# Performance work log

Hardware: AMD Instinct MI355X
Metric: run time of the kernel (lower is better)

## Reference

```python
import jax, jax.numpy as jnp
import numpy as np

B, L, D_IN = 32, 200, 64
H = 64          # hidden_size
A = 36          # attention_size
NEG_SLOPE = 0.01  # torch LeakyReLU default


def setup_inputs() -> dict:
    key = jax.random.key(0)
    ks = jax.random.split(key, 7)
    s_ln = 1.0 / np.sqrt(D_IN)
    s_w1 = 1.0 / np.sqrt(3 * H)
    s_w2 = 1.0 / np.sqrt(A)
    return {
        "x": jax.random.normal(ks[0], (B, L, D_IN), dtype=jnp.float32),
        "ln_w": jax.random.uniform(ks[1], (D_IN, H), minval=-s_ln, maxval=s_ln, dtype=jnp.float32),
        "ln_b": jax.random.uniform(ks[2], (H,), minval=-s_ln, maxval=s_ln, dtype=jnp.float32),
        "w1": jax.random.uniform(ks[3], (3 * H, A), minval=-s_w1, maxval=s_w1, dtype=jnp.float32),
        "b1": jax.random.uniform(ks[4], (A,), minval=-s_w1, maxval=s_w1, dtype=jnp.float32),
        "w2": jax.random.uniform(ks[5], (A,), minval=-s_w2, maxval=s_w2, dtype=jnp.float32),
        "b2": jax.random.uniform(ks[6], (), minval=-s_w2, maxval=s_w2, dtype=jnp.float32),
    }


def reference(x, ln_w, ln_b, w1, b1, w2, b2):
    # x: [B, L, D_in] -> h: [B, L, H]
    h = jnp.einsum("bld,dh->blh", x, ln_w) + ln_b
    Ld = h.shape[1]
    Hd = h.shape[-1]
    # The torch code concatenates (x1, x2, x1*x2) where x1[b,i,j]=h[b,j],
    # x2[b,i,j]=h[b,i]. Split w1 accordingly instead of materializing the
    # [B,L,L,3H] concat tensor.
    w1a, w1b, w1c = w1[:Hd], w1[Hd:2 * Hd], w1[2 * Hd:]
    a = jnp.einsum("bjh,ha->bja", h, w1a)          # x1 contribution (depends on j)
    c = jnp.einsum("bih,ha->bia", h, w1b)          # x2 contribution (depends on i)
    cross = jnp.einsum("bih,bjh,ha->bija", h, h, w1c)  # (x1*x2) contribution
    pre = a[:, None, :, :] + c[:, :, None, :] + cross + b1   # [B,L,L,A]
    act = jax.nn.leaky_relu(pre, negative_slope=NEG_SLOPE)
    score = jnp.einsum("bija,a->bij", act, w2) + b2          # [B,L,L]
    mask = jnp.tril(jnp.ones((Ld, Ld), dtype=score.dtype))   # causal (incl. diag)
    score = score * mask
    return jnp.einsum("bij,bjh->bih", score, h)               # [B,L,H]
```

## Files before the change

kernel.cpp:

```cpp
#include <hip/hip_runtime.h>

#define B 32
#define L 200
#define DIN 64
#define H 64
#define A 36

typedef __attribute__((ext_vector_type(8))) short short8;
typedef __attribute__((ext_vector_type(4))) float floatx4;
typedef __attribute__((ext_vector_type(8))) float floatx8;

static __device__ __forceinline__ short f2bf(float f) {
    union { float f; unsigned u; } v; v.f = f;
    unsigned r = (v.u + 0x7FFF + ((v.u >> 16) & 1)) >> 16;
    return (short)r;
}

__global__ __launch_bounds__(256) void prep_kernel(
    const float* __restrict__ x, const float* __restrict__ ln_w,
    const float* __restrict__ ln_b, const float* __restrict__ w1,
    float* __restrict__ h_out, float* __restrict__ cc_out, short* __restrict__ hb16_out,
    float* __restrict__ w1a_r, float* __restrict__ w1c_r)
{
    int wave = threadIdx.x >> 6;
    int lane = threadIdx.x & 63;
    int bl = __builtin_amdgcn_readfirstlane(blockIdx.x * 4 + wave);
    const float* xr = x + (size_t)bl * DIN;
    float p0 = ln_b[lane], p1 = 0.f;
    #pragma unroll
    for (int d = 0; d < DIN; d += 2) {
        p0 = fmaf(xr[d],     ln_w[d * H + lane],       p0);
        p1 = fmaf(xr[d + 1], ln_w[(d + 1) * H + lane], p1);
    }
    float acc = p0 + p1;
    __shared__ float hrow[4][H];
    hrow[wave][lane] = acc;
    h_out[(size_t)bl * H + lane] = acc;
    int j = bl % L;
    hb16_out[(size_t)bl * H + (lane ^ ((j & 7) << 3))] = f2bf(acc);
    if (lane < A) {
        float s0 = 0.f, s1 = 0.f;
        #pragma unroll
        for (int hh = 0; hh < H; hh += 2) {
            s0 = fmaf(hrow[wave][hh],     w1[(H + hh) * A + lane],     s0);
            s1 = fmaf(hrow[wave][hh + 1], w1[(H + hh + 1) * A + lane], s1);
        }
        cc_out[(size_t)bl * A + lane] = s0 + s1;
    }
    if (blockIdx.x == 0) {
        for (int idx = threadIdx.x; idx < 2 * 3 * 64 * 8; idx += 256) {
            int e = idx & 7, ln = (idx >> 3) & 63, sn = idx >> 9;
            int s = sn / 3, n = sn - 3 * s;
            int k = s * 32 + (ln >> 4) * 8 + e;
            int c = n * 16 + (ln & 15);
            w1a_r[idx] = (c < A) ? w1[k * A + c] : 0.f;
            w1c_r[idx] = (c < A) ? w1[(2 * H + k) * A + c] : 0.f;
        }
    }
}

__global__ __launch_bounds__(256) void score_kernel(
    const float* __restrict__ h, const short* __restrict__ hb16,
    const float* __restrict__ cc, const float* __restrict__ w1a_r,
    const float* __restrict__ w1c_r, const float* __restrict__ b1,
    const float* __restrict__ w2, const float* __restrict__ b2,
    float* __restrict__ out)
{
    int blk = blockIdx.x;
    int b  = blk / 50;
    int bg = blk - b * 50;
    int wave = threadIdx.x >> 6;
    int lane = threadIdx.x & 63;
    int i = __builtin_amdgcn_readfirstlane(bg + 50 * wave);
    int l15 = lane & 15, l4 = lane >> 4;

    __shared__ __align__(16) short tile[208 * 64];

    const short* hb16b = hb16 + (size_t)b * L * H;

    for (int c = wave; c < 26; c += 4) {
        int j = (c < 25) ? (c * 8 + (lane >> 3)) : (L - 1);
        const short* src = hb16b + (size_t)j * H + (lane & 7) * 8;
        __builtin_amdgcn_global_load_lds(
            (const __attribute__((address_space(1))) void*)src,
            (__attribute__((address_space(3))) void*)&tile[c * 512],
            16, 0, 0);
    }

    const float* hi    = h + ((size_t)b * L + i) * H;
    const float* ccrow = cc + ((size_t)b * L + i) * A;
    float b2v = b2[0];
    float w2v[3][4], cbv[3][4];
    #pragma unroll
    for (int n = 0; n < 3; ++n) {
        #pragma unroll
        for (int r = 0; r < 4; ++r) {
            int a = n * 16 + l4 * 4 + r;
            bool av = a < A;
            w2v[n][r] = av ? w2[a] : 0.f;
            cbv[n][r] = av ? (ccrow[a] + b1[a]) : 0.f;
        }
    }
    short8 afrag[2][3];
    #pragma unroll
    for (int s = 0; s < 2; ++s) {
        float hik[8];
        #pragma unroll
        for (int e = 0; e < 8; ++e) hik[e] = hi[s * 32 + l4 * 8 + e];
        #pragma unroll
        for (int n = 0; n < 3; ++n) {
            floatx8 wa = *(const floatx8*)&w1a_r[(((s * 3 + n) * 64) + lane) * 8];
            floatx8 wc = *(const floatx8*)&w1c_r[(((s * 3 + n) * 64) + lane) * 8];
            #pragma unroll
            for (int e = 0; e < 8; ++e)
                afrag[s][n][e] = f2bf(fmaf(hik[e], wc[e], wa[e]));
        }
    }
    __syncthreads();

    float oacc[4] = {0.f, 0.f, 0.f, 0.f};
    int mmax = (i >> 4) + 1;

    for (int m = 0; m < mmax; ++m) {
        int row = m * 16 + l15;
        const short* brow = tile + row * 64;
        int sw = (l15 & 7) << 3;
        short8 bf0 = *(const short8*)(brow + ((l4 * 8) ^ sw));
        short8 bf1 = *(const short8*)(brow + ((32 + l4 * 8) ^ sw));
        floatx4 c0 = {cbv[0][0], cbv[0][1], cbv[0][2], cbv[0][3]};
        floatx4 c1 = {cbv[1][0], cbv[1][1], cbv[1][2], cbv[1][3]};
        floatx4 c2 = {cbv[2][0], cbv[2][1], cbv[2][2], cbv[2][3]};
        c0 = __builtin_amdgcn_mfma_f32_16x16x32_bf16(afrag[0][0], bf0, c0, 0, 0, 0);
        c1 = __builtin_amdgcn_mfma_f32_16x16x32_bf16(afrag[0][1], bf0, c1, 0, 0, 0);
        c2 = __builtin_amdgcn_mfma_f32_16x16x32_bf16(afrag[0][2], bf0, c2, 0, 0, 0);
        c0 = __builtin_amdgcn_mfma_f32_16x16x32_bf16(afrag[1][0], bf1, c0, 0, 0, 0);
        c1 = __builtin_amdgcn_mfma_f32_16x16x32_bf16(afrag[1][1], bf1, c1, 0, 0, 0);
        c2 = __builtin_amdgcn_mfma_f32_16x16x32_bf16(afrag[1][2], bf1, c2, 0, 0, 0);
        float sp0 = 0.f, sp1 = 0.f, sp2 = 0.f;
        #pragma unroll
        for (int r = 0; r < 4; ++r) {
            sp0 = fmaf(fmaxf(c0[r], 0.01f * c0[r]), w2v[0][r], sp0);
            sp1 = fmaf(fmaxf(c1[r], 0.01f * c1[r]), w2v[1][r], sp1);
            sp2 = fmaf(fmaxf(c2[r], 0.01f * c2[r]), w2v[2][r], sp2);
        }
        float sp = (sp0 + sp1) + sp2;
        sp += __shfl_xor(sp, 16, 64);
        sp += __shfl_xor(sp, 32, 64);
        float sc = (row <= i) ? sp + b2v : 0.f;

        const float* hjb = h + ((size_t)b * L + m * 16) * H + lane;
        #pragma unroll
        for (int rb = 0; rb < 4; ++rb) {
            #pragma unroll
            for (int q = 0; q < 4; ++q) {
                int jq = rb * 4 + q;
                float sq = __int_as_float(
                    __builtin_amdgcn_readlane(__float_as_int(sc), jq));
                float hv = hjb[jq * H];
                oacc[rb] = fmaf(sq, hv, oacc[rb]);
            }
        }
    }

    out[((size_t)b * L + i) * H + lane] = (oacc[0] + oacc[1]) + (oacc[2] + oacc[3]);
}

extern "C" void kernel_launch(void* const* d_in, const int* in_sizes, int n_in,
                              void* d_out, int out_size, void* d_ws, size_t ws_size,
                              hipStream_t stream) {
    const float* x    = (const float*)d_in[0];
    const float* ln_w = (const float*)d_in[1];
    const float* ln_b = (const float*)d_in[2];
    const float* w1   = (const float*)d_in[3];
    const float* b1   = (const float*)d_in[4];
    const float* w2   = (const float*)d_in[5];
    const float* b2   = (const float*)d_in[6];
    float* out = (float*)d_out;

    float* h_ws   = (float*)d_ws;
    float* cc_ws  = h_ws + (size_t)B * L * H;
    short* hb16_ws = (short*)(cc_ws + (size_t)B * L * A);
    float* w1a_r  = (float*)(hb16_ws + (size_t)B * L * H);
    float* w1c_r  = w1a_r + 3072;

    prep_kernel<<<(B * L) / 4, 256, 0, stream>>>(x, ln_w, ln_b, w1, h_ws, cc_ws,
                                                 hb16_ws, w1a_r, w1c_r);
    score_kernel<<<B * 50, 256, 0, stream>>>(h_ws, hb16_ws, cc_ws, w1a_r, w1c_r,
                                             b1, w2, b2, out);
}
```

Measured before the change: 37.69 us.

## Pair causal rows i and 199-i per wave to balance triangular work

Each wave now handles two query rows, i1 and its mirror 199-i1, so every wave does roughly the same amount of causal work. The grid shrinks from 1600 to 800 blocks. The LDS tile staging is trimmed to the rows the block actually needs, and the bf16 tile load is amortized over two rows per wave. The cost is fewer blocks to spread across CUs and the two phases running serially inside each wave.

```diff
diff --git a/kernel.cpp b/kernel.cpp
--- a/kernel.cpp
+++ b/kernel.cpp
@@ -67,19 +67,23 @@
     float* __restrict__ out)
 {
     int blk = blockIdx.x;
-    int b  = blk / 50;
-    int bg = blk - b * 50;
+    int b  = blk / 25;
+    int bg = blk - b * 25;
     int wave = threadIdx.x >> 6;
     int lane = threadIdx.x & 63;
-    int i = __builtin_amdgcn_readfirstlane(bg + 50 * wave);
+    int i1 = __builtin_amdgcn_readfirstlane(bg * 4 + wave);
+    int i2 = 199 - i1;
     int l15 = lane & 15, l4 = lane >> 4;
 
     __shared__ __align__(16) short tile[208 * 64];
 
     const short* hb16b = hb16 + (size_t)b * L * H;
-
-    for (int c = wave; c < 26; c += 4) {
-        int j = (c < 25) ? (c * 8 + (lane >> 3)) : (L - 1);
+    const float* h_b   = h + (size_t)b * L * H;
+
+    int i2max = 199 - 4 * bg;
+    int nch = (((i2max | 15) + 1) + 7) >> 3;
+    for (int c = wave; c < nch; c += 4) {
+        int j = c * 8 + (lane >> 3); if (j > L - 1) j = L - 1;
         const short* src = hb16b + (size_t)j * H + (lane & 7) * 8;
         __builtin_amdgcn_global_load_lds(
             (const __attribute__((address_space(1))) void*)src,
@@ -87,82 +91,94 @@
             16, 0, 0);
     }
 
-    const float* hi    = h + ((size_t)b * L + i) * H;
-    const float* ccrow = cc + ((size_t)b * L + i) * A;
     float b2v = b2[0];
-    float w2v[3][4], cbv[3][4];
+    float w2v[3][4];
     #pragma unroll
     for (int n = 0; n < 3; ++n) {
         #pragma unroll
         for (int r = 0; r < 4; ++r) {
             int a = n * 16 + l4 * 4 + r;
-            bool av = a < A;
-            w2v[n][r] = av ? w2[a] : 0.f;
-            cbv[n][r] = av ? (ccrow[a] + b1[a]) : 0.f;
-        }
-    }
-    short8 afrag[2][3];
-    #pragma unroll
-    for (int s = 0; s < 2; ++s) {
-        float hik[8];
-        #pragma unroll
-        for (int e = 0; e < 8; ++e) hik[e] = hi[s * 32 + l4 * 8 + e];
-        #pragma unroll
-        for (int n = 0; n < 3; ++n) {
-            floatx8 wa = *(const floatx8*)&w1a_r[(((s * 3 + n) * 64) + lane) * 8];
-            floatx8 wc = *(const floatx8*)&w1c_r[(((s * 3 + n) * 64) + lane) * 8];
-            #pragma unroll
-            for (int e = 0; e < 8; ++e)
-                afrag[s][n][e] = f2bf(fmaf(hik[e], wc[e], wa[e]));
-        }
-    }
-    __syncthreads();
-
-    float oacc[4] = {0.f, 0.f, 0.f, 0.f};
-    int mmax = (i >> 4) + 1;
-
-    for (int m = 0; m < mmax; ++m) {
-        int row = m * 16 + l15;
-        const short* brow = tile + row * 64;
-        int sw = (l15 & 7) << 3;
-        short8 bf0 = *(const short8*)(brow + ((l4 * 8) ^ sw));
-        short8 bf1 = *(const short8*)(brow + ((32 + l4 * 8) ^ sw));
-        floatx4 c0 = {cbv[0][0], cbv[0][1], cbv[0][2], cbv[0][3]};
-        floatx4 c1 = {cbv[1][0], cbv[1][1], cbv[1][2], cbv[1][3]};
-        floatx4 c2 = {cbv[2][0], cbv[2][1], cbv[2][2], cbv[2][3]};
-        c0 = __builtin_amdgcn_mfma_f32_16x16x32_bf16(afrag[0][0], bf0, c0, 0, 0, 0);
-        c1 = __builtin_amdgcn_mfma_f32_16x16x32_bf16(afrag[0][1], bf0, c1, 0, 0, 0);
-        c2 = __builtin_amdgcn_mfma_f32_16x16x32_bf16(afrag[0][2], bf0, c2, 0, 0, 0);
-        c0 = __builtin_amdgcn_mfma_f32_16x16x32_bf16(afrag[1][0], bf1, c0, 0, 0, 0);
-        c1 = __builtin_amdgcn_mfma_f32_16x16x32_bf16(afrag[1][1], bf1, c1, 0, 0, 0);
-        c2 = __builtin_amdgcn_mfma_f32_16x16x32_bf16(afrag[1][2], bf1, c2, 0, 0, 0);
-        float sp0 = 0.f, sp1 = 0.f, sp2 = 0.f;
-        #pragma unroll
-        for (int r = 0; r < 4; ++r) {
-            sp0 = fmaf(fmaxf(c0[r], 0.01f * c0[r]), w2v[0][r], sp0);
-            sp1 = fmaf(fmaxf(c1[r], 0.01f * c1[r]), w2v[1][r], sp1);
-            sp2 = fmaf(fmaxf(c2[r], 0.01f * c2[r]), w2v[2][r], sp2);
-        }
-        float sp = (sp0 + sp1) + sp2;
-        sp += __shfl_xor(sp, 16, 64);
-        sp += __shfl_xor(sp, 32, 64);
-        float sc = (row <= i) ? sp + b2v : 0.f;
-
-        const float* hjb = h + ((size_t)b * L + m * 16) * H + lane;
-        #pragma unroll
-        for (int rb = 0; rb < 4; ++rb) {
-            #pragma unroll
-            for (int q = 0; q < 4; ++q) {
-                int jq = rb * 4 + q;
-                float sq = __int_as_float(
-                    __builtin_amdgcn_readlane(__float_as_int(sc), jq));
-                float hv = hjb[jq * H];
-                oacc[rb] = fmaf(sq, hv, oacc[rb]);
-            }
-        }
-    }
-
-    out[((size_t)b * L + i) * H + lane] = (oacc[0] + oacc[1]) + (oacc[2] + oacc[3]);
+            w2v[n][r] = (a < A) ? w2[a] : 0.f;
+        }
+    }
+
+    #pragma unroll 1
+    for (int ph = 0; ph < 2; ++ph) {
+        int i = __builtin_amdgcn_readfirstlane(ph ? i1 : i2);
+
+        const float* hi    = h_b + (size_t)i * H;
+        const float* ccrow = cc + ((size_t)b * L + i) * A;
+        float cbv[3][4];
+        #pragma unroll
+        for (int n = 0; n < 3; ++n)
+            #pragma unroll
+            for (int r = 0; r < 4; ++r) {
+                int a = n * 16 + l4 * 4 + r;
+                cbv[n][r] = (a < A) ? (ccrow[a] + b1[a]) : 0.f;
+            }
+        short8 afrag[2][3];
+        #pragma unroll
+        for (int s = 0; s < 2; ++s) {
+            float hik[8];
+            #pragma unroll
+            for (int e = 0; e < 8; ++e) hik[e] = hi[s * 32 + l4 * 8 + e];
+            #pragma unroll
+            for (int n = 0; n < 3; ++n) {
+                floatx8 wa = *(const floatx8*)&w1a_r[(((s * 3 + n) * 64) + lane) * 8];
+                floatx8 wc = *(const floatx8*)&w1c_r[(((s * 3 + n) * 64) + lane) * 8];
+                #pragma unroll
+                for (int e = 0; e < 8; ++e)
+                    afrag[s][n][e] = f2bf(fmaf(hik[e], wc[e], wa[e]));
+            }
+        }
+        if (ph == 0) __syncthreads();
+
+        float oacc[4] = {0.f, 0.f, 0.f, 0.f};
+        int mmax = (i >> 4) + 1;
+
+        for (int m = 0; m < mmax; ++m) {
+            int row = m * 16 + l15;
+            const short* brow = tile + row * 64;
+            int sw = (l15 & 7) << 3;
+            short8 bf0 = *(const short8*)(brow + ((l4 * 8) ^ sw));
+            short8 bf1 = *(const short8*)(brow + ((32 + l4 * 8) ^ sw));
+            floatx4 c0 = {cbv[0][0], cbv[0][1], cbv[0][2], cbv[0][3]};
+            floatx4 c1 = {cbv[1][0], cbv[1][1], cbv[1][2], cbv[1][3]};
+            floatx4 c2 = {cbv[2][0], cbv[2][1], cbv[2][2], cbv[2][3]};
+            c0 = __builtin_amdgcn_mfma_f32_16x16x32_bf16(afrag[0][0], bf0, c0, 0, 0, 0);
+            c1 = __builtin_amdgcn_mfma_f32_16x16x32_bf16(afrag[0][1], bf0, c1, 0, 0, 0);
+            c2 = __builtin_amdgcn_mfma_f32_16x16x32_bf16(afrag[0][2], bf0, c2, 0, 0, 0);
+            c0 = __builtin_amdgcn_mfma_f32_16x16x32_bf16(afrag[1][0], bf1, c0, 0, 0, 0);
+            c1 = __builtin_amdgcn_mfma_f32_16x16x32_bf16(afrag[1][1], bf1, c1, 0, 0, 0);
+            c2 = __builtin_amdgcn_mfma_f32_16x16x32_bf16(afrag[1][2], bf1, c2, 0, 0, 0);
+            float sp0 = 0.f, sp1 = 0.f, sp2 = 0.f;
+            #pragma unroll
+            for (int r = 0; r < 4; ++r) {
+                sp0 = fmaf(fmaxf(c0[r], 0.01f * c0[r]), w2v[0][r], sp0);
+                sp1 = fmaf(fmaxf(c1[r], 0.01f * c1[r]), w2v[1][r], sp1);
+                sp2 = fmaf(fmaxf(c2[r], 0.01f * c2[r]), w2v[2][r], sp2);
+            }
+            float sp = (sp0 + sp1) + sp2;
+            sp += __shfl_xor(sp, 16, 64);
+            sp += __shfl_xor(sp, 32, 64);
+            float sc = (row <= i) ? sp + b2v : 0.f;
+
+            const float* hjb = h_b + (size_t)(m * 16) * H + lane;
+            #pragma unroll
+            for (int rb = 0; rb < 4; ++rb) {
+                #pragma unroll
+                for (int q = 0; q < 4; ++q) {
+                    int jq = rb * 4 + q;
+                    float sq = __int_as_float(
+                        __builtin_amdgcn_readlane(__float_as_int(sc), jq));
+                    float hv = hjb[jq * H];
+                    oacc[rb] = fmaf(sq, hv, oacc[rb]);
+                }
+            }
+        }
+
+        out[((size_t)b * L + i) * H + lane] = (oacc[0] + oacc[1]) + (oacc[2] + oacc[3]);
+    }
 }
 
 extern "C" void kernel_launch(void* const* d_in, const int* in_sizes, int n_in,
@@ -185,6 +201,6 @@
 
     prep_kernel<<<(B * L) / 4, 256, 0, stream>>>(x, ln_w, ln_b, w1, h_ws, cc_ws,
                                                  hb16_ws, w1a_r, w1c_r);
-    score_kernel<<<B * 50, 256, 0, stream>>>(h_ws, hb16_ws, cc_ws, w1a_r, w1c_r,
+    score_kernel<<<B * 25, 256, 0, stream>>>(h_ws, hb16_ws, cc_ws, w1a_r, w1c_r,
                                              b1, w2, b2, out);
 }
```

New measurement: 39.29 us. 4.2% more time.

## Fuse projection into score kernel, recompute h per block via MFMA in LDS

Applied to the files above, without the earlier changes.

Merges the prep and score kernels into one launch. Each block recomputes the bf16 h rows it needs with MFMA straight into swizzled LDS, and computes the per-row c projection in-kernel. It also reads h_j for the output accumulation from LDS in bf16 instead of fp32 global memory. Rows are regrouped so each block handles four consecutive i, with the heaviest blocks scheduled first. This removes a kernel launch and the global round-trip of h/cc, at the cost of redundant recompute of h per block and extra bf16 rounding of h (including x rounded to bf16) in the final weighted sum.

```diff
diff --git a/kernel.cpp b/kernel.cpp
--- a/kernel.cpp
+++ b/kernel.cpp
@@ -15,108 +15,100 @@
     unsigned r = (v.u + 0x7FFF + ((v.u >> 16) & 1)) >> 16;
     return (short)r;
 }
+static __device__ __forceinline__ float bf2f(short s) {
+    union { unsigned u; float f; } v; v.u = ((unsigned)(unsigned short)s) << 16;
+    return v.f;
+}
 
-__global__ __launch_bounds__(256) void prep_kernel(
+__global__ __launch_bounds__(256) void fused_kernel(
     const float* __restrict__ x, const float* __restrict__ ln_w,
     const float* __restrict__ ln_b, const float* __restrict__ w1,
-    float* __restrict__ h_out, float* __restrict__ cc_out, short* __restrict__ hb16_out,
-    float* __restrict__ w1a_r, float* __restrict__ w1c_r)
-{
-    int wave = threadIdx.x >> 6;
-    int lane = threadIdx.x & 63;
-    int bl = __builtin_amdgcn_readfirstlane(blockIdx.x * 4 + wave);
-    const float* xr = x + (size_t)bl * DIN;
-    float p0 = ln_b[lane], p1 = 0.f;
-    #pragma unroll
-    for (int d = 0; d < DIN; d += 2) {
-        p0 = fmaf(xr[d],     ln_w[d * H + lane],       p0);
-        p1 = fmaf(xr[d + 1], ln_w[(d + 1) * H + lane], p1);
-    }
-    float acc = p0 + p1;
-    __shared__ float hrow[4][H];
-    hrow[wave][lane] = acc;
-    h_out[(size_t)bl * H + lane] = acc;
-    int j = bl % L;
-    hb16_out[(size_t)bl * H + (lane ^ ((j & 7) << 3))] = f2bf(acc);
-    if (lane < A) {
-        float s0 = 0.f, s1 = 0.f;
-        #pragma unroll
-        for (int hh = 0; hh < H; hh += 2) {
-            s0 = fmaf(hrow[wave][hh],     w1[(H + hh) * A + lane],     s0);
-            s1 = fmaf(hrow[wave][hh + 1], w1[(H + hh + 1) * A + lane], s1);
-        }
-        cc_out[(size_t)bl * A + lane] = s0 + s1;
-    }
-    if (blockIdx.x == 0) {
-        for (int idx = threadIdx.x; idx < 2 * 3 * 64 * 8; idx += 256) {
-            int e = idx & 7, ln = (idx >> 3) & 63, sn = idx >> 9;
-            int s = sn / 3, n = sn - 3 * s;
-            int k = s * 32 + (ln >> 4) * 8 + e;
-            int c = n * 16 + (ln & 15);
-            w1a_r[idx] = (c < A) ? w1[k * A + c] : 0.f;
-            w1c_r[idx] = (c < A) ? w1[(2 * H + k) * A + c] : 0.f;
-        }
-    }
-}
-
-__global__ __launch_bounds__(256) void score_kernel(
-    const float* __restrict__ h, const short* __restrict__ hb16,
-    const float* __restrict__ cc, const float* __restrict__ w1a_r,
-    const float* __restrict__ w1c_r, const float* __restrict__ b1,
-    const float* __restrict__ w2, const float* __restrict__ b2,
-    float* __restrict__ out)
+    const float* __restrict__ b1, const float* __restrict__ w2,
+    const float* __restrict__ b2, float* __restrict__ out)
 {
     int blk = blockIdx.x;
     int b  = blk / 50;
-    int bg = blk - b * 50;
+    int g  = 49 - (blk - b * 50);
     int wave = threadIdx.x >> 6;
     int lane = threadIdx.x & 63;
-    int i = __builtin_amdgcn_readfirstlane(bg + 50 * wave);
+    int i = __builtin_amdgcn_readfirstlane(g * 4 + wave);
     int l15 = lane & 15, l4 = lane >> 4;
+    int MT = ((4 * g + 3) >> 4) + 1;
 
     __shared__ __align__(16) short tile[208 * 64];
 
-    const short* hb16b = hb16 + (size_t)b * L * H;
+    const float* xb = x + (size_t)b * L * DIN;
 
-    for (int c = wave; c < 26; c += 4) {
-        int j = (c < 25) ? (c * 8 + (lane >> 3)) : (L - 1);
-        const short* src = hb16b + (size_t)j * H + (lane & 7) * 8;
-        __builtin_amdgcn_global_load_lds(
-            (const __attribute__((address_space(1))) void*)src,
-            (__attribute__((address_space(3))) void*)&tile[c * 512],
-            16, 0, 0);
+    for (int n = 0; n < 4; ++n) {
+        floatx4 lnb = *(const floatx4*)(ln_b + n * 16 + l4 * 4);
+        short8 af[2];
+        #pragma unroll
+        for (int s = 0; s < 2; ++s)
+            #pragma unroll
+            for (int e = 0; e < 8; ++e)
+                af[s][e] = f2bf(ln_w[(s * 32 + l4 * 8 + e) * H + n * 16 + l15]);
+        for (int mt = wave; mt < MT; mt += 4) {
+            int row = mt * 16 + l15;
+            int rj = row > L - 1 ? L - 1 : row;
+            short8 xf[2];
+            #pragma unroll
+            for (int s = 0; s < 2; ++s) {
+                floatx8 xv = *(const floatx8*)(xb + (size_t)rj * DIN + s * 32 + l4 * 8);
+                #pragma unroll
+                for (int e = 0; e < 8; ++e) xf[s][e] = f2bf(xv[e]);
+            }
+            floatx4 c = lnb;
+            c = __builtin_amdgcn_mfma_f32_16x16x32_bf16(af[0], xf[0], c, 0, 0, 0);
+            c = __builtin_amdgcn_mfma_f32_16x16x32_bf16(af[1], xf[1], c, 0, 0, 0);
+            unsigned p0 = (unsigned short)f2bf(c[0]) | ((unsigned)(unsigned short)f2bf(c[1]) << 16);
+            unsigned p1 = (unsigned short)f2bf(c[2]) | ((unsigned)(unsigned short)f2bf(c[3]) << 16);
+            int byte = row * 128 + ((n * 32 + l4 * 8) ^ ((row & 7) << 4));
+            uint2 pv; pv.x = p0; pv.y = p1;
+            *(uint2*)((char*)tile + byte) = pv;
+        }
     }
+    __syncthreads();
 
-    const float* hi    = h + ((size_t)b * L + i) * H;
-    const float* ccrow = cc + ((size_t)b * L + i) * A;
+    float hval = bf2f(tile[i * 64 + (lane ^ ((i & 7) << 3))]);
+    float cb = (lane < A) ? b1[lane] : 0.f;
+    const float* w1b = w1 + (size_t)H * A;
+    #pragma unroll 8
+    for (int k = 0; k < H; ++k) {
+        float hk = __int_as_float(
+            __builtin_amdgcn_readlane(__float_as_int(hval), k));
+        cb = fmaf(hk, w1b[k * A + lane], cb);
+    }
     float b2v = b2[0];
-    float w2v[3][4], cbv[3][4];
+    float cbv[3][4], w2v[3][4];
     #pragma unroll
-    for (int n = 0; n < 3; ++n) {
+    for (int n = 0; n < 3; ++n)
         #pragma unroll
         for (int r = 0; r < 4; ++r) {
             int a = n * 16 + l4 * 4 + r;
-            bool av = a < A;
-            w2v[n][r] = av ? w2[a] : 0.f;
-            cbv[n][r] = av ? (ccrow[a] + b1[a]) : 0.f;
+            float v = __shfl(cb, a, 64);
+            cbv[n][r] = (a < A) ? v : 0.f;
+            w2v[n][r] = (a < A) ? w2[a] : 0.f;
         }
-    }
     short8 afrag[2][3];
     #pragma unroll
     for (int s = 0; s < 2; ++s) {
+        short8 hraw = *(const short8*)(tile + i * 64 + ((s * 32 + l4 * 8) ^ ((i & 7) << 3)));
         float hik[8];
         #pragma unroll
-        for (int e = 0; e < 8; ++e) hik[e] = hi[s * 32 + l4 * 8 + e];
+        for (int e = 0; e < 8; ++e) hik[e] = bf2f(hraw[e]);
         #pragma unroll
         for (int n = 0; n < 3; ++n) {
-            floatx8 wa = *(const floatx8*)&w1a_r[(((s * 3 + n) * 64) + lane) * 8];
-            floatx8 wc = *(const floatx8*)&w1c_r[(((s * 3 + n) * 64) + lane) * 8];
+            int c = n * 16 + l15;
+            bool cv = c < A;
             #pragma unroll
-            for (int e = 0; e < 8; ++e)
-                afrag[s][n][e] = f2bf(fmaf(hik[e], wc[e], wa[e]));
+            for (int e = 0; e < 8; ++e) {
+                int k = s * 32 + l4 * 8 + e;
+                float wa = cv ? w1[k * A + c] : 0.f;
+                float wc = cv ? w1[(2 * H + k) * A + c] : 0.f;
+                afrag[s][n][e] = f2bf(fmaf(hik[e], wc, wa));
+            }
         }
     }
-    __syncthreads();
 
     float oacc[4] = {0.f, 0.f, 0.f, 0.f};
     int mmax = (i >> 4) + 1;
@@ -148,15 +140,15 @@
         sp += __shfl_xor(sp, 32, 64);
         float sc = (row <= i) ? sp + b2v : 0.f;
 
-        const float* hjb = h + ((size_t)b * L + m * 16) * H + lane;
         #pragma unroll
         for (int rb = 0; rb < 4; ++rb) {
             #pragma unroll
             for (int q = 0; q < 4; ++q) {
                 int jq = rb * 4 + q;
+                int jr = m * 16 + jq;
                 float sq = __int_as_float(
                     __builtin_amdgcn_readlane(__float_as_int(sc), jq));
-                float hv = hjb[jq * H];
+                float hv = bf2f(tile[jr * 64 + (lane ^ ((jr & 7) << 3))]);
                 oacc[rb] = fmaf(sq, hv, oacc[rb]);
             }
         }
@@ -177,14 +169,5 @@
     const float* b2   = (const float*)d_in[6];
     float* out = (float*)d_out;
 
-    float* h_ws   = (float*)d_ws;
-    float* cc_ws  = h_ws + (size_t)B * L * H;
-    short* hb16_ws = (short*)(cc_ws + (size_t)B * L * A);
-    float* w1a_r  = (float*)(hb16_ws + (size_t)B * L * H);
-    float* w1c_r  = w1a_r + 3072;
-
-    prep_kernel<<<(B * L) / 4, 256, 0, stream>>>(x, ln_w, ln_b, w1, h_ws, cc_ws,
-                                                 hb16_ws, w1a_r, w1c_r);
-    score_kernel<<<B * 50, 256, 0, stream>>>(h_ws, hb16_ws, cc_ws, w1a_r, w1c_r,
-                                             b1, w2, b2, out);
+    fused_kernel<<<B * 50, 256, 0, stream>>>(x, ln_w, ln_b, w1, b1, w2, b2, out);
 }
```

New measurement: 60.26 us. 59.9% more time.

## Split tile staging into two phases and load only needed causal rows

Applied to the files above, without the earlier changes.

The score kernel now stages the first 64 bf16 h rows into LDS before the barrier. It loads the remaining rows, only up to the block's maximum causal row, after that barrier, so those loads overlap with compute on the first four 16-row chunks. A second barrier separates the phases. Block order is reversed so blocks with longer causal ranges start first, and the per-lane cc/b1/w2 gathers are replaced by one coalesced load plus wave shuffles. This adds a second barrier, and the shuffles add some latency.

```diff
diff --git a/kernel.cpp b/kernel.cpp
--- a/kernel.cpp
+++ b/kernel.cpp
@@ -68,7 +68,7 @@
 {
     int blk = blockIdx.x;
     int b  = blk / 50;
-    int bg = blk - b * 50;
+    int bg = 49 - (blk - b * 50);
     int wave = threadIdx.x >> 6;
     int lane = threadIdx.x & 63;
     int i = __builtin_amdgcn_readfirstlane(bg + 50 * wave);
@@ -77,9 +77,12 @@
     __shared__ __align__(16) short tile[208 * 64];
 
     const short* hb16b = hb16 + (size_t)b * L * H;
-
-    for (int c = wave; c < 26; c += 4) {
-        int j = (c < 25) ? (c * 8 + (lane >> 3)) : (L - 1);
+    const float* h_b   = h + (size_t)b * L * H;
+
+    int maxrow = bg + 150;
+    int nch = (((maxrow | 15) + 1) + 7) >> 3;
+    for (int c = wave; c < 8; c += 4) {
+        int j = c * 8 + (lane >> 3);
         const short* src = hb16b + (size_t)j * H + (lane & 7) * 8;
         __builtin_amdgcn_global_load_lds(
             (const __attribute__((address_space(1))) void*)src,
@@ -87,18 +90,18 @@
             16, 0, 0);
     }
 
-    const float* hi    = h + ((size_t)b * L + i) * H;
-    const float* ccrow = cc + ((size_t)b * L + i) * A;
+    const float* hi = h_b + (size_t)i * H;
     float b2v = b2[0];
+    float ccl = (lane < A) ? (cc[((size_t)b * L + i) * A + lane] + b1[lane]) : 0.f;
+    float w2l = (lane < A) ? w2[lane] : 0.f;
     float w2v[3][4], cbv[3][4];
     #pragma unroll
     for (int n = 0; n < 3; ++n) {
         #pragma unroll
         for (int r = 0; r < 4; ++r) {
             int a = n * 16 + l4 * 4 + r;
-            bool av = a < A;
-            w2v[n][r] = av ? w2[a] : 0.f;
-            cbv[n][r] = av ? (ccrow[a] + b1[a]) : 0.f;
+            cbv[n][r] = __shfl(ccl, a, 64);
+            w2v[n][r] = __shfl(w2l, a, 64);
         }
     }
     short8 afrag[2][3];
@@ -118,48 +121,64 @@
     }
     __syncthreads();
 
+    for (int c = 8 + wave; c < nch; c += 4) {
+        int j = c * 8 + (lane >> 3); if (j > L - 1) j = L - 1;
+        const short* src = hb16b + (size_t)j * H + (lane & 7) * 8;
+        __builtin_amdgcn_global_load_lds(
+            (const __attribute__((address_space(1))) void*)src,
+            (__attribute__((address_space(3))) void*)&tile[c * 512],
+            16, 0, 0);
+    }
+
     float oacc[4] = {0.f, 0.f, 0.f, 0.f};
     int mmax = (i >> 4) + 1;
-
-    for (int m = 0; m < mmax; ++m) {
-        int row = m * 16 + l15;
-        const short* brow = tile + row * 64;
-        int sw = (l15 & 7) << 3;
-        short8 bf0 = *(const short8*)(brow + ((l4 * 8) ^ sw));
-        short8 bf1 = *(const short8*)(brow + ((32 + l4 * 8) ^ sw));
-        floatx4 c0 = {cbv[0][0], cbv[0][1], cbv[0][2], cbv[0][3]};
-        floatx4 c1 = {cbv[1][0], cbv[1][1], cbv[1][2], cbv[1][3]};
-        floatx4 c2 = {cbv[2][0], cbv[2][1], cbv[2][2], cbv[2][3]};
-        c0 = __builtin_amdgcn_mfma_f32_16x16x32_bf16(afrag[0][0], bf0, c0, 0, 0, 0);
-        c1 = __builtin_amdgcn_mfma_f32_16x16x32_bf16(afrag[0][1], bf0, c1, 0, 0, 0);
-        c2 = __builtin_amdgcn_mfma_f32_16x16x32_bf16(afrag[0][2], bf0, c2, 0, 0, 0);
-        c0 = __builtin_amdgcn_mfma_f32_16x16x32_bf16(afrag[1][0], bf1, c0, 0, 0, 0);
-        c1 = __builtin_amdgcn_mfma_f32_16x16x32_bf16(afrag[1][1], bf1, c1, 0, 0, 0);
-        c2 = __builtin_amdgcn_mfma_f32_16x16x32_bf16(afrag[1][2], bf1, c2, 0, 0, 0);
-        float sp0 = 0.f, sp1 = 0.f, sp2 = 0.f;
-        #pragma unroll
-        for (int r = 0; r < 4; ++r) {
-            sp0 = fmaf(fmaxf(c0[r], 0.01f * c0[r]), w2v[0][r], sp0);
-            sp1 = fmaf(fmaxf(c1[r], 0.01f * c1[r]), w2v[1][r], sp1);
-            sp2 = fmaf(fmaxf(c2[r], 0.01f * c2[r]), w2v[2][r], sp2);
-        }
-        float sp = (sp0 + sp1) + sp2;
-        sp += __shfl_xor(sp, 16, 64);
-        sp += __shfl_xor(sp, 32, 64);
-        float sc = (row <= i) ? sp + b2v : 0.f;
-
-        const float* hjb = h + ((size_t)b * L + m * 16) * H + lane;
-        #pragma unroll
-        for (int rb = 0; rb < 4; ++rb) {
+    int mlim1 = mmax < 4 ? mmax : 4;
+
+    #pragma unroll 1
+    for (int phase = 0; phase < 2; ++phase) {
+        int m0   = phase ? 4 : 0;
+        int mend = phase ? mmax : mlim1;
+        for (int m = m0; m < mend; ++m) {
+            int row = m * 16 + l15;
+            const short* brow = tile + row * 64;
+            int sw = (l15 & 7) << 3;
+            short8 bf0 = *(const short8*)(brow + ((l4 * 8) ^ sw));
+            short8 bf1 = *(const short8*)(brow + ((32 + l4 * 8) ^ sw));
+            floatx4 c0 = {cbv[0][0], cbv[0][1], cbv[0][2], cbv[0][3]};
+            floatx4 c1 = {cbv[1][0], cbv[1][1], cbv[1][2], cbv[1][3]};
+            floatx4 c2 = {cbv[2][0], cbv[2][1], cbv[2][2], cbv[2][3]};
+            c0 = __builtin_amdgcn_mfma_f32_16x16x32_bf16(afrag[0][0], bf0, c0, 0, 0, 0);
+            c1 = __builtin_amdgcn_mfma_f32_16x16x32_bf16(afrag[0][1], bf0, c1, 0, 0, 0);
+            c2 = __builtin_amdgcn_mfma_f32_16x16x32_bf16(afrag[0][2], bf0, c2, 0, 0, 0);
+            c0 = __builtin_amdgcn_mfma_f32_16x16x32_bf16(afrag[1][0], bf1, c0, 0, 0, 0);
+            c1 = __builtin_amdgcn_mfma_f32_16x16x32_bf16(afrag[1][1], bf1, c1, 0, 0, 0);
+            c2 = __builtin_amdgcn_mfma_f32_16x16x32_bf16(afrag[1][2], bf1, c2, 0, 0, 0);
+            float sp0 = 0.f, sp1 = 0.f, sp2 = 0.f;
             #pragma unroll
-            for (int q = 0; q < 4; ++q) {
-                int jq = rb * 4 + q;
-                float sq = __int_as_float(
-                    __builtin_amdgcn_readlane(__float_as_int(sc), jq));
-                float hv = hjb[jq * H];
-                oacc[rb] = fmaf(sq, hv, oacc[rb]);
+            for (int r = 0; r < 4; ++r) {
+                sp0 = fmaf(fmaxf(c0[r], 0.01f * c0[r]), w2v[0][r], sp0);
+                sp1 = fmaf(fmaxf(c1[r], 0.01f * c1[r]), w2v[1][r], sp1);
+                sp2 = fmaf(fmaxf(c2[r], 0.01f * c2[r]), w2v[2][r], sp2);
             }
-        }
+            float sp = (sp0 + sp1) + sp2;
+            sp += __shfl_xor(sp, 16, 64);
+            sp += __shfl_xor(sp, 32, 64);
+            float sc = (row <= i) ? sp + b2v : 0.f;
+
+            const float* hjb = h_b + (size_t)(m * 16) * H + lane;
+            #pragma unroll
+            for (int rb = 0; rb < 4; ++rb) {
+                #pragma unroll
+                for (int q = 0; q < 4; ++q) {
+                    int jq = rb * 4 + q;
+                    float sq = __int_as_float(
+                        __builtin_amdgcn_readlane(__float_as_int(sc), jq));
+                    float hv = hjb[jq * H];
+                    oacc[rb] = fmaf(sq, hv, oacc[rb]);
+                }
+            }
+        }
+        if (phase == 0) __syncthreads();
     }
 
     out[((size_t)b * L + i) * H + lane] = (oacc[0] + oacc[1]) + (oacc[2] + oacc[3]);
```

Result: slower. 45.32 us (+20.3%).
